# Kernel optimization log

Measured on AMD Instinct MI355X. Metric: run time of the kernel, lower is better.

Reference implementation:

```python
import jax, jax.numpy as jnp
import numpy as np

# 3x3 Gaussian smoothing kernel (symmetric, so correlation == convolution)
GAUSS = jnp.array([[1., 2., 1.], [2., 4., 2.], [1., 2., 1.]], dtype=jnp.float32) / 16.0


def _per_sample_conv_valid(x, k):
    """Per-sample 3x3 cross-correlation. x: [B,H,W], k: [B,3,3] -> [B,H-2,W-2].

    Implemented as a grouped conv treating batch as channels (groups=B),
    matching F.conv2d(pred.permute(1,0,2,3), weight=k[:,None], groups=B).
    """
    B = x.shape[0]
    out = jax.lax.conv_general_dilated(
        x[None],            # [1, B, H, W]
        k[:, None],         # [B, 1, 3, 3]
        window_strides=(1, 1), padding='VALID',
        dimension_numbers=('NCHW', 'OIHW', 'NCHW'),
        feature_group_count=B)
    return out[0]


def _gauss_blur_same(x):
    """SAME-padded 3x3 Gaussian smoothing. x: [B,h,w] -> [B,h,w]."""
    out = jax.lax.conv_general_dilated(
        x[:, None],                 # [B,1,h,w]
        GAUSS[None, None],          # [1,1,3,3]
        window_strides=(1, 1), padding='SAME',
        dimension_numbers=('NCHW', 'OIHW', 'NCHW'))
    return out[:, 0]


def setup_inputs() -> dict:
    key = jax.random.key(0)
    k1, k2, k3, k4 = jax.random.split(key, 4)
    B, H, W = 256, 256, 256
    pred = jax.random.normal(k1, (B, H, W), dtype=jnp.float32)
    rhs = jax.random.normal(k2, (B, H - 2, W - 2), dtype=jnp.float32)
    Laplace_kernel = jax.random.normal(k3, (B, 3, 3), dtype=jnp.float32)
    Df_dr_kernel = jax.random.normal(k4, (B, 3, 3), dtype=jnp.float32)
    RR = jnp.arange(B * H * W, dtype=jnp.float32).reshape(B, H, W)
    ZZ = jnp.arange(B * H * W, dtype=jnp.float32).reshape(B, H, W)
    return {"pred": pred, "rhs": rhs, "Laplace_kernel": Laplace_kernel,
            "Df_dr_kernel": Df_dr_kernel, "RR": RR, "ZZ": ZZ}


def reference(pred, rhs, Laplace_kernel, Df_dr_kernel, RR, ZZ):
    # Finite-difference Grad-Shafranov operator (per-sample stencils).
    Lpsi = _per_sample_conv_valid(pred, Laplace_kernel)          # [B,H-2,W-2]
    Dpsi_dr = -_per_sample_conv_valid(pred, Df_dr_kernel)        # [B,H-2,W-2]
    RR_in = RR[:, 1:-1, 1:-1]
    Dpsi_dr = Dpsi_dr / RR_in
    GS_ope = Lpsi - Dpsi_dr

    # Grid spacings and normalization alfa / (hr^2 * hz^2)
    hr = RR[:, 1, 2] - RR[:, 1, 1]                               # [B]
    hz = ZZ[:, 2, 1] - ZZ[:, 1, 1]                               # [B]
    alfa = -2.0 * (hr ** 2 + hz ** 2)
    scale = (alfa / (hr ** 2 * hz ** 2))[:, None, None]
    GS_ope = GS_ope * scale

    # Gaussian smoothing then MSE against rhs
    GS_ope = _gauss_blur_same(GS_ope)
    return jnp.mean((GS_ope - rhs) ** 2)
```

## Files before the change

kernel.cpp:

```cpp
#include <hip/hip_runtime.h>

#define HW 256
#define OW 254
#define RSTRIP 8
#define NITER (RSTRIP + 2)
#define NBLOCK 2048
#define NOUT (256.0f * 254.0f * 254.0f)

__device__ __forceinline__ void load_row8(const float* __restrict__ base, int row,
                                          int cL, int c0, int cB, float* p) {
    p[0] = base[row * HW + cL];
    float4 v0 = *(const float4*)&base[row * HW + c0];
    p[1] = v0.x; p[2] = v0.y; p[3] = v0.z; p[4] = v0.w;
    float4 v1 = *(const float4*)&base[row * HW + cB];
    p[5] = v1.x; p[6] = v1.y; p[7] = v1.z;
}

__device__ __forceinline__ void load_rr6(const float* __restrict__ RRb, int row,
                                         int c0, float* rq) {
    float4 q0 = *(const float4*)&RRb[row * HW + c0];
    rq[0] = q0.x; rq[1] = q0.y; rq[2] = q0.z; rq[3] = q0.w;
    float2 q1 = *(const float2*)&RRb[row * HW + c0 + 4];
    rq[4] = q1.x; rq[5] = q1.y;
}

__device__ __forceinline__ void load_rhs4v(const float* __restrict__ rhsb, int row,
                                           int c0, int c2, float* rh) {
    float2 a = *(const float2*)&rhsb[row * OW + c0];
    float2 b = *(const float2*)&rhsb[row * OW + c2];
    rh[0] = a.x; rh[1] = a.y; rh[2] = b.x; rh[3] = b.y;
}

__device__ __forceinline__ float uniformf(float x) {
    return __int_as_float(__builtin_amdgcn_readfirstlane(__float_as_int(x)));
}

__global__ __launch_bounds__(256) void pde_loss_main(
    const float* __restrict__ pred, const float* __restrict__ rhs,
    const float* __restrict__ Lk,   const float* __restrict__ Dk,
    const float* __restrict__ RR,   const float* __restrict__ ZZ,
    float* __restrict__ partial)
{
    const int tid  = threadIdx.x;
    const int lane = tid & 63;
    const int wv   = tid >> 6;
    const int gw   = blockIdx.x * 4 + wv;
    const int b    = gw >> 5;
    const int strip= gw & 31;
    const int r0   = strip * RSTRIP;
    const int r1   = min(r0 + RSTRIP, OW);

    const float* predb = pred + (size_t)b * (HW * HW);
    const float* RRb   = RR   + (size_t)b * (HW * HW);
    const float* ZZb   = ZZ   + (size_t)b * (HW * HW);
    const float* rhsb  = rhs  + (size_t)b * (OW * OW);

    float kl[9], kd[9];
    #pragma unroll
    for (int q = 0; q < 9; q++) {
        kl[q] = uniformf(Lk[b * 9 + q]);
        kd[q] = uniformf(Dk[b * 9 + q]);
    }
    float hr = RRb[1 * HW + 2] - RRb[1 * HW + 1];
    float hz = ZZb[2 * HW + 1] - ZZb[1 * HW + 1];
    float hr2 = hr * hr, hz2 = hz * hz;
    const float scale = uniformf((-2.0f * (hr2 + hz2)) / (hr2 * hz2));

    const int c0 = lane * 4;
    const int cL = max(c0 - 1, 0);
    const int cB = min(c0 + 4, HW - 4);
    const int c2 = min(c0 + 2, OW - 4);

    float pA[8], pB[8];
    load_row8(predb, max(r0 - 1, 0), cL, c0, cB, pA);
    load_row8(predb, r0,             cL, c0, cB, pB);

    float P[4] = {0, 0, 0, 0};
    float Q[4] = {0, 0, 0, 0};
    float acc = 0.0f;

    #pragma unroll
    for (int s = 0; s < NITER; ++s) {
        const int g = r0 - 1 + s;

        float pC[8], rq[6], rh[4];
        load_row8(predb, min(g + 2, HW - 1), cL, c0, cB, pC);
        load_rr6 (RRb,  min(max(g + 1, 1), HW - 2), c0, rq);
        load_rhs4v(rhsb, min(max(g - 1, 0), OW - 1), c0, c2, rh);

        const bool rowok = (g >= 0) && (g < OW);
        float gs[6];
        #pragma unroll
        for (int u = 0; u < 6; ++u) {
            float sL = 0.0f, sD = 0.0f;
            #pragma unroll
            for (int kx = 0; kx < 3; ++kx) {
                sL = fmaf(pA[u + kx], kl[kx],     sL);
                sL = fmaf(pB[u + kx], kl[3 + kx], sL);
                sL = fmaf(pC[u + kx], kl[6 + kx], sL);
                sD = fmaf(pA[u + kx], kd[kx],     sD);
                sD = fmaf(pB[u + kx], kd[3 + kx], sD);
                sD = fmaf(pC[u + kx], kd[6 + kx], sD);
            }
            float gval = scale * fmaf(sD, __builtin_amdgcn_rcpf(rq[u]), sL);
            int x = c0 - 1 + u;
            gs[u] = (rowok && x >= 0 && x < OW) ? gval : 0.0f;
        }

        float hb[4];
        #pragma unroll
        for (int t = 0; t < 4; ++t)
            hb[t] = gs[t] + 2.0f * gs[t + 1] + gs[t + 2];

        const int i = g - 1;
        const bool iok = (s >= 2) && (i < r1);
        #pragma unroll
        for (int t = 0; t < 4; ++t) {
            float F = (P[t] + hb[t]) * (1.0f / 16.0f);
            float d = F - rh[t];
            acc += (iok && (c0 + t) < OW) ? d * d : 0.0f;
        }

        #pragma unroll
        for (int t = 0; t < 4; ++t) {
            P[t] = Q[t] + 2.0f * hb[t];
            Q[t] = hb[t];
        }
        #pragma unroll
        for (int t = 0; t < 8; ++t) { pA[t] = pB[t]; pB[t] = pC[t]; }
    }

    #pragma unroll
    for (int off = 32; off > 0; off >>= 1)
        acc += __shfl_down(acc, off, 64);
    __shared__ float sw[4];
    if (lane == 0) sw[wv] = acc;
    __syncthreads();
    if (tid == 0)
        partial[blockIdx.x] = sw[0] + sw[1] + sw[2] + sw[3];
}

__global__ __launch_bounds__(256) void pde_loss_reduce(
    const float* __restrict__ partial, int n, float* __restrict__ out)
{
    float acc = 0.0f;
    for (int i = threadIdx.x; i < n; i += 256) acc += partial[i];
    #pragma unroll
    for (int off = 32; off > 0; off >>= 1)
        acc += __shfl_down(acc, off, 64);
    __shared__ float sw[4];
    if ((threadIdx.x & 63) == 0) sw[threadIdx.x >> 6] = acc;
    __syncthreads();
    if (threadIdx.x == 0)
        out[0] = (sw[0] + sw[1] + sw[2] + sw[3]) / NOUT;
}

extern "C" void kernel_launch(void* const* d_in, const int* in_sizes, int n_in,
                              void* d_out, int out_size, void* d_ws, size_t ws_size,
                              hipStream_t stream) {
    const float* pred = (const float*)d_in[0];
    const float* rhs  = (const float*)d_in[1];
    const float* Lk   = (const float*)d_in[2];
    const float* Dk   = (const float*)d_in[3];
    const float* RR   = (const float*)d_in[4];
    const float* ZZ   = (const float*)d_in[5];
    float* out = (float*)d_out;
    float* partial = (float*)d_ws;

    pde_loss_main<<<NBLOCK, 256, 0, stream>>>(pred, rhs, Lk, Dk, RR, ZZ, partial);
    pde_loss_reduce<<<1, 256, 0, stream>>>(partial, NBLOCK, out);
}
```

Before: 234.6 us.

## Preload all strip rows upfront and shrink strips to six rows

```diff
diff --git a/kernel.cpp b/kernel.cpp
--- a/kernel.cpp
+++ b/kernel.cpp
@@ -2,9 +2,11 @@
 
 #define HW 256
 #define OW 254
-#define RSTRIP 8
-#define NITER (RSTRIP + 2)
-#define NBLOCK 2048
+#define RSTRIP 6
+#define NSTRIPS 43
+#define NWAVES (256 * NSTRIPS)
+#define NBLOCK (NWAVES / 4)
+#define NGS (RSTRIP + 2)
 #define NOUT (256.0f * 254.0f * 254.0f)
 
 __device__ __forceinline__ void load_row8(const float* __restrict__ base, int row,
@@ -35,7 +37,7 @@
     return __int_as_float(__builtin_amdgcn_readfirstlane(__float_as_int(x)));
 }
 
-__global__ __launch_bounds__(256) void pde_loss_main(
+__global__ __launch_bounds__(256, 1) void pde_loss_main(
     const float* __restrict__ pred, const float* __restrict__ rhs,
     const float* __restrict__ Lk,   const float* __restrict__ Dk,
     const float* __restrict__ RR,   const float* __restrict__ ZZ,
@@ -45,8 +47,8 @@
     const int lane = tid & 63;
     const int wv   = tid >> 6;
     const int gw   = blockIdx.x * 4 + wv;
-    const int b    = gw >> 5;
-    const int strip= gw & 31;
+    const int b    = gw / NSTRIPS;
+    const int strip= gw - b * NSTRIPS;
     const int r0   = strip * RSTRIP;
     const int r1   = min(r0 + RSTRIP, OW);
 
@@ -71,38 +73,44 @@
     const int cB = min(c0 + 4, HW - 4);
     const int c2 = min(c0 + 2, OW - 4);
 
-    float pA[8], pB[8];
-    load_row8(predb, max(r0 - 1, 0), cL, c0, cB, pA);
-    load_row8(predb, r0,             cL, c0, cB, pB);
+    float p[NGS + 2][8];
+    #pragma unroll
+    for (int s = 0; s < NGS + 2; ++s)
+        load_row8(predb, min(max(r0 - 1 + s, 0), HW - 1), cL, c0, cB, p[s]);
+    float rq[NGS][6];
+    #pragma unroll
+    for (int s = 0; s < NGS; ++s)
+        load_rr6(RRb, min(max(r0 + s, 1), HW - 2), c0, rq[s]);
+    float rh[RSTRIP][4];
+    #pragma unroll
+    for (int s = 0; s < RSTRIP; ++s)
+        load_rhs4v(rhsb, min(r0 + s, OW - 1), c0, c2, rh[s]);
+
+    __builtin_amdgcn_sched_barrier(0);
 
     float P[4] = {0, 0, 0, 0};
     float Q[4] = {0, 0, 0, 0};
     float acc = 0.0f;
 
     #pragma unroll
-    for (int s = 0; s < NITER; ++s) {
+    for (int s = 0; s < NGS; ++s) {
         const int g = r0 - 1 + s;
+        const bool rowok = (g >= 0) && (g < OW);
 
-        float pC[8], rq[6], rh[4];
-        load_row8(predb, min(g + 2, HW - 1), cL, c0, cB, pC);
-        load_rr6 (RRb,  min(max(g + 1, 1), HW - 2), c0, rq);
-        load_rhs4v(rhsb, min(max(g - 1, 0), OW - 1), c0, c2, rh);
-
-        const bool rowok = (g >= 0) && (g < OW);
         float gs[6];
         #pragma unroll
         for (int u = 0; u < 6; ++u) {
             float sL = 0.0f, sD = 0.0f;
             #pragma unroll
             for (int kx = 0; kx < 3; ++kx) {
-                sL = fmaf(pA[u + kx], kl[kx],     sL);
-                sL = fmaf(pB[u + kx], kl[3 + kx], sL);
-                sL = fmaf(pC[u + kx], kl[6 + kx], sL);
-                sD = fmaf(pA[u + kx], kd[kx],     sD);
-                sD = fmaf(pB[u + kx], kd[3 + kx], sD);
-                sD = fmaf(pC[u + kx], kd[6 + kx], sD);
+                sL = fmaf(p[s][u + kx],     kl[kx],     sL);
+                sL = fmaf(p[s + 1][u + kx], kl[3 + kx], sL);
+                sL = fmaf(p[s + 2][u + kx], kl[6 + kx], sL);
+                sD = fmaf(p[s][u + kx],     kd[kx],     sD);
+                sD = fmaf(p[s + 1][u + kx], kd[3 + kx], sD);
+                sD = fmaf(p[s + 2][u + kx], kd[6 + kx], sD);
             }
-            float gval = scale * fmaf(sD, __builtin_amdgcn_rcpf(rq[u]), sL);
+            float gval = scale * fmaf(sD, __builtin_amdgcn_rcpf(rq[s][u]), sL);
             int x = c0 - 1 + u;
             gs[u] = (rowok && x >= 0 && x < OW) ? gval : 0.0f;
         }
@@ -114,10 +122,11 @@
 
         const int i = g - 1;
         const bool iok = (s >= 2) && (i < r1);
+        const float* rhrow = rh[(s >= 2) ? (s - 2) : 0];
         #pragma unroll
         for (int t = 0; t < 4; ++t) {
             float F = (P[t] + hb[t]) * (1.0f / 16.0f);
-            float d = F - rh[t];
+            float d = F - rhrow[t];
             acc += (iok && (c0 + t) < OW) ? d * d : 0.0f;
         }
 
@@ -126,8 +135,6 @@
             P[t] = Q[t] + 2.0f * hb[t];
             Q[t] = hb[t];
         }
-        #pragma unroll
-        for (int t = 0; t < 8; ++t) { pA[t] = pB[t]; pB[t] = pC[t]; }
     }
 
     #pragma unroll
```

After: 226.0 us. -3.7%, faster.
